# Performance work log

Measured on AMD Instinct MI355X. Metric: run time of the kernel, lower is better.

Reference implementation:

```python
import jax, jax.numpy as jnp
import numpy as np

STU, ITEM, CONC, D = 50000, 20000, 2000, 128
E_CC, E_IC, E_SI = 40000, 80000, 1000000


def _gat(tgt_x, src_x, e_src, e_dst, n_tgt, W, att_l, att_r, slope=0.2):
    # single-head GATConv, aggr='add', concat with heads=1 -> [n_tgt, D]
    if W is not None:
        xl = src_x @ W.T  # lin_l applied to source
        xr = tgt_x @ W.T  # lin_l shared for target (in_channels is int)
        # noqa: torch module uses lin_l for both when in_channels is int
    else:
        xl, xr = src_x, tgt_x
    sl = xl @ att_l  # [n_src]
    sr = xr @ att_r  # [n_tgt]
    e = sl[e_src] + sr[e_dst]
    e = jnp.where(e > 0, e, slope * e)  # leaky_relu
    # segment softmax over edges grouped by target node
    m = jax.ops.segment_max(e, e_dst, num_segments=n_tgt)
    m = jnp.where(jnp.isfinite(m), m, 0.0)
    ex = jnp.exp(e - m[e_dst])
    den = jax.ops.segment_sum(ex, e_dst, num_segments=n_tgt) + 1e-16
    alpha = ex / den[e_dst]
    return jax.ops.segment_sum(xl[e_src] * alpha[:, None], e_dst, num_segments=n_tgt)


def setup_inputs():
    key = jax.random.key(0)
    ks = jax.random.split(key, 40)
    s = 1.0 / np.sqrt(D)
    n = lambda k, sh, sc=1.0: jax.random.normal(k, sh, jnp.float32) * sc
    return {
        'stu_x': n(ks[0], (STU, D)),
        'item_x': n(ks[1], (ITEM, D)),
        'conc_x': n(ks[2], (CONC, D)),
        'stu_raw_x': n(ks[3], (STU, D)),
        'W_cc': n(ks[4], (D, D), s), 'al_cc': n(ks[5], (D,), s), 'ar_cc': n(ks[6], (D,), s),
        'W_ic': n(ks[7], (D, D), s), 'al_ic': n(ks[8], (D,), s), 'ar_ic': n(ks[9], (D,), s),
        'al_cce': n(ks[10], (D,), s), 'ar_cce': n(ks[11], (D,), s),
        'al_ice': n(ks[12], (D,), s), 'ar_ice': n(ks[13], (D,), s),
        'W_ci': n(ks[14], (D, D), s), 'al_ci': n(ks[15], (D,), s), 'ar_ci': n(ks[16], (D,), s),
        'W_si': n(ks[17], (D, D), s), 'al_si': n(ks[18], (D,), s), 'ar_si': n(ks[19], (D,), s),
        'w_ci_att': n(ks[20], (2 * D,), s), 'w_si_att': n(ks[21], (2 * D,), s),
        'W_is': n(ks[22], (D, D), s), 'al_is': n(ks[23], (D,), s), 'ar_is': n(ks[24], (D,), s),
        'cc_src': jax.random.randint(ks[25], (E_CC,), 0, CONC),
        'cc_dst': jax.random.randint(ks[26], (E_CC,), 0, CONC),
        'ic_item': jax.random.randint(ks[27], (E_IC,), 0, ITEM),
        'ic_conc': jax.random.randint(ks[28], (E_IC,), 0, CONC),
        'si_stu': jax.random.randint(ks[29], (E_SI,), 0, STU),
        'si_item': jax.random.randint(ks[30], (E_SI,), 0, ITEM),
    }


def reference(stu_x, item_x, conc_x, stu_raw_x,
              W_cc, al_cc, ar_cc, W_ic, al_ic, ar_ic,
              al_cce, ar_cce, al_ice, ar_ice,
              W_ci, al_ci, ar_ci, W_si, al_si, ar_si,
              w_ci_att, w_si_att, W_is, al_is, ar_is,
              cc_src, cc_dst, ic_item, ic_conc, si_stu, si_item):
    # --- concept fusion ---
    c1 = _gat(conc_x, conc_x, cc_src, cc_dst, CONC, W_cc, al_cc, ar_cc)   # inter_conc_conc
    c2 = _gat(conc_x, item_x, ic_item, ic_conc, CONC, W_ic, al_ic, ar_ic) # inter_item_conc
    e1 = _gat(conc_x, c1, cc_src, cc_dst, CONC, None, al_cce, ar_cce)     # exter_conc_conc (no lin)
    e2 = _gat(conc_x, c2, cc_src, cc_dst, CONC, None, al_ice, ar_ice)     # exter_item_conc (no lin)
    conc_fused = conc_x + e1 + e2
    # --- item fusion ---
    i1 = _gat(item_x, conc_x, ic_conc, ic_item, ITEM, W_ci, al_ci, ar_ci) # inter_conc_item
    i2 = _gat(item_x, stu_x, si_stu, si_item, ITEM, W_si, al_si, ar_si)   # inter_stu_item
    # softmax over dim=1 of an [N,1] tensor (as in the torch code): equals 1.0
    att1 = jax.nn.softmax((jnp.concatenate([i1, item_x], axis=1) @ w_ci_att)[:, None], axis=1)
    att2 = jax.nn.softmax((jnp.concatenate([i2, item_x], axis=1) @ w_si_att)[:, None], axis=1)
    item_fused = item_x + att1 * i1 + att2 * i2
    # --- student fusion (uses raw data['stu'].x as target) ---
    s1 = _gat(stu_raw_x, item_x, si_item, si_stu, STU, W_is, al_is, ar_is)
    stu_fused = stu_raw_x + s1
    return (conc_fused, item_fused, stu_fused)
```

## Files before the change

kernel.cpp:

```cpp
#include <hip/hip_runtime.h>

#define CONC_N 2000
#define ITEM_N 20000
#define STU_N  50000
#define NE_CC  40000
#define NE_IC  80000
#define NE_SI  1000000
#define TBUCK  382

typedef unsigned int uint;
typedef unsigned short ushort;
typedef signed char s8;
typedef __attribute__((ext_vector_type(8))) short bf16x8;
typedef __attribute__((ext_vector_type(4))) float f32x4;

__device__ __forceinline__ ushort f2bf(float f) {
  uint u = __float_as_uint(f);
  uint r = (u + 0x7FFFu + ((u >> 16) & 1u)) >> 16;
  return (ushort)r;
}

__device__ __forceinline__ bf16x8 packfrag(float4 lo, float4 hi) {
  union { bf16x8 s; uint u[4]; } p;
  p.u[0] = (uint)f2bf(lo.x) | ((uint)f2bf(lo.y) << 16);
  p.u[1] = (uint)f2bf(lo.z) | ((uint)f2bf(lo.w) << 16);
  p.u[2] = (uint)f2bf(hi.x) | ((uint)f2bf(hi.y) << 16);
  p.u[3] = (uint)f2bf(hi.z) | ((uint)f2bf(hi.w) << 16);
  return p.s;
}


struct CsrG {
  const int* dst; const int* src;
  unsigned* keys; int* srcs; int* offs;
  int E, n, shift, nbuck, tb, sb;
};
struct CsrGs { CsrG g[5]; };


struct ProjDesc { const float* W; const float* a; float* out; };
struct SetupArgs {
  ProjDesc p[10];
  CsrGs G;
  int* pcnt;
  const float* wsrc[5];
  ushort* wdst[5];
};

__global__ __launch_bounds__(256) void setup_k(SetupArgs A) {
  int b = blockIdx.x;
  int tid = threadIdx.x;
  if (b < 10) {
    __shared__ float Wl[128 * 132];
    __shared__ float a_s[128];
    ProjDesc d = A.p[b];
    #pragma unroll
    for (int i = 0; i < 16; ++i) {
      int s = tid + i * 256;
      int row = s >> 5, c4 = s & 31;
      float4 w = *(const float4*)&d.W[s * 4];
      float* dst = &Wl[row * 132 + c4 * 4];
      dst[0] = w.x; dst[1] = w.y; dst[2] = w.z; dst[3] = w.w;
    }
    if (tid < 128) a_s[tid] = d.a[tid];
    __syncthreads();
    if (tid < 128) {
      float acc = 0.f;
      #pragma unroll 4
      for (int j = 0; j < 128; ++j) acc += Wl[j * 132 + tid] * a_s[j];
      d.out[tid] = acc;
    }
    return;
  }
  if (b >= 170) {
    int wi = b - 170;
    const float* Ws = A.wsrc[wi];
    ushort* Wd = A.wdst[wi];
    for (int rec = tid; rec < 2048; rec += 256) {
      int lane = rec & 63;
      int kk = (rec >> 6) & 3;
      int nt = rec >> 8;
      int x = lane & 15, g = lane >> 4;
      const float* src = &Ws[(nt * 16 + x) * 128 + kk * 32 + 4 * g];
      float4 lo = *(const float4*)src;
      float4 hi = *(const float4*)(src + 16);
      bf16x8 pk = packfrag(lo, hi);
      *(bf16x8*)&Wd[rec * 8] = pk;
    }
    return;
  }
  int bsel = b - 10;
  int gi = bsel >> 5, blk = bsel & 31;
  CsrG g = A.G.g[gi];
  __shared__ int lcnt[128];
  if (tid < 128) lcnt[tid] = 0;
  __syncthreads();
  int chunk = (g.E + 31) >> 5;
  int e0 = blk * chunk, e1 = min(g.E, e0 + chunk);
  for (int e = e0 + tid; e < e1; e += 256)
    atomicAdd(&lcnt[g.dst[e] >> g.shift], 1);
  __syncthreads();
  if (tid < 128) A.pcnt[bsel * 128 + tid] = lcnt[tid];
}


__global__ __launch_bounds__(512) void csr_scan(CsrGs G, const int* __restrict__ pcnt,
                                                int* __restrict__ cur, int* __restrict__ bases) {
  __shared__ int lc[TBUCK];
  __shared__ int lb[TBUCK + 5];
  int tid = threadIdx.x, lane = tid & 63, wv = tid >> 6;
  if (tid < TBUCK) {
    int gi = 0;
    #pragma unroll
    for (int k = 1; k < 5; ++k) if (tid >= G.g[k].tb) gi = k;
    int b = tid - G.g[gi].tb;
    int s = 0;
    for (int blk = 0; blk < 32; ++blk) s += pcnt[((gi << 5) + blk) * 128 + b];
    lc[tid] = s;
  }
  __syncthreads();
  if (wv < 5) {
    CsrG g = G.g[wv];
    int carry = 0;
    for (int base = 0; base < g.nbuck; base += 64) {
      int idx = base + lane;
      int v = (idx < g.nbuck) ? lc[g.tb + idx] : 0;
      int incl = v;
      #pragma unroll
      for (int o = 1; o < 64; o <<= 1) {
        int y = __shfl_up(incl, o);
        if (lane >= o) incl += y;
      }
      if (idx < g.nbuck) lb[g.sb + idx] = carry + incl - v;
      carry += __shfl(incl, 63);
    }
    if (lane == 0) lb[g.sb + g.nbuck] = carry;
  }
  __syncthreads();
  if (tid < TBUCK + 5) bases[tid] = lb[tid];
  if (tid < TBUCK) {
    int gi = 0;
    for (int k = 1; k < 5; ++k) if (tid >= G.g[k].tb) gi = k;
    cur[tid] = lb[tid + gi];
  }
  if (tid < 5) G.g[tid].offs[G.g[tid].n] = G.g[tid].E;
}


__device__ void partition_body(const CsrGs& G, int* __restrict__ cur, int gi, int bx,
                               int nbx, unsigned char* smem) {
  CsrG g = G.g[gi];
  unsigned* ck = (unsigned*)smem;
  unsigned char* cb = smem + 16384;
  int* lcnt = (int*)(smem + 20480);
  int* lcur = (int*)(smem + 20992);
  int tid = threadIdx.x;
  unsigned dmask = (1u << g.shift) - 1;
  for (int c0 = bx * 4096; c0 < g.E; c0 += nbx * 4096) {
    if (tid < 128) lcnt[tid] = 0;
    __syncthreads();
    #pragma unroll
    for (int i = 0; i < 16; ++i) {
      int e = c0 + i * 256 + tid;
      if (e < g.E) {
        int d = g.dst[e], s = g.src[e];
        int b = d >> g.shift;
        ck[i * 256 + tid] = ((unsigned)(d & dmask) << 16) | (unsigned)s;
        cb[i * 256 + tid] = (unsigned char)b;
        atomicAdd(&lcnt[b], 1);
      } else cb[i * 256 + tid] = 255;
    }
    __syncthreads();
    if (tid < g.nbuck && lcnt[tid] > 0) lcur[tid] = atomicAdd(&cur[g.tb + tid], lcnt[tid]);
    __syncthreads();
    #pragma unroll
    for (int i = 0; i < 16; ++i) {
      int b = cb[i * 256 + tid];
      if (b != 255) {
        int pos = atomicAdd(&lcur[b], 1);
        g.keys[pos] = ck[i * 256 + tid];
      }
    }
    __syncthreads();
  }
}

__device__ void rdot_body(const float* __restrict__ x, const float* __restrict__ v,
                          float* __restrict__ o, int n, int blk, int nblk) {
  int lane = threadIdx.x & 63;
  int wid = (blk * 256 + threadIdx.x) >> 6;
  int nw = nblk * 4;
  float va = v[lane], vb = v[64 + lane];
  for (int r = wid; r < n; r += nw) {
    float a = x[r * 128 + lane] * va + x[r * 128 + 64 + lane] * vb;
    #pragma unroll
    for (int of = 32; of; of >>= 1) a += __shfl_xor(a, of);
    if (lane == 0) o[r] = a;
  }
}

__global__ __launch_bounds__(256) void mid3_k(CsrGs G, int* cur,
                                              const float* rx, const float* rv,
                                              float* ro, int rnb) {
  __shared__ __align__(16) unsigned char smem[21504];
  int b = blockIdx.x;
  if (b < 600) {
    partition_body(G, cur, b / 120, b % 120, 120, smem);
  } else {
    rdot_body(rx, rv, ro, STU_N, b - 600, rnb);
  }
}


struct GemmDesc { const float* X; s8* Y8; float* S; int n, b0;
                  const float* dv[6]; float* dq[6]; };
struct BigC {
  GemmDesc g[5];
  int gemm_blocks;
};

__device__ void build_lite(const CsrGs& G, const int* __restrict__ bases, int bid,
                           int* lh, int* lex, int* lcu, int* wsum) {
  int gi = 0;
  for (int k = 1; k < 5; ++k) if (bid >= G.g[k].tb) gi = k;
  CsrG g = G.g[gi];
  int b = bid - g.tb;
  int base = bases[g.sb + b];
  int cnt = bases[g.sb + b + 1] - base;

  int tid = threadIdx.x;
  lh[tid] = 0; lh[tid + 256] = 0;
  __syncthreads();
  for (int j = tid; j < cnt; j += 256)
    atomicAdd(&lh[g.keys[base + j] >> 16], 1);
  __syncthreads();
  int a0 = lh[2 * tid], a1 = lh[2 * tid + 1];
  int pair = a0 + a1;
  int lane = tid & 63, wv = tid >> 6;
  int incl = pair;
  #pragma unroll
  for (int o = 1; o < 64; o <<= 1) {
    int y = __shfl_up(incl, o);
    if (lane >= o) incl += y;
  }
  if (lane == 63) wsum[wv] = incl;
  __syncthreads();
  if (tid == 0) {
    int s = 0;
    #pragma unroll
    for (int w = 0; w < 4; ++w) { int t = wsum[w]; wsum[w] = s; s += t; }
  }
  __syncthreads();
  int ep = wsum[wv] + incl - pair;
  lex[2 * tid] = ep;       lex[2 * tid + 1] = ep + a0;
  lcu[2 * tid] = ep;       lcu[2 * tid + 1] = ep + a0;
  __syncthreads();
  int dst0 = b << g.shift;
  int ndst = min(1 << g.shift, g.n - dst0);
  for (int dl = tid; dl < ndst; dl += 256) g.offs[dst0 + dl] = base + lex[dl];
  for (int j = tid; j < cnt; j += 256) {
    unsigned k = g.keys[base + j];
    int dl = k >> 16;
    int pos = atomicAdd(&lcu[dl], 1);
    g.srcs[base + pos] = (int)(k & 0xFFFFu);
  }
}

template <int NV>
__device__ void gemm_bodyT(const GemmDesc& gd, const ushort* __restrict__ Wf, int blk) {
  int tid = threadIdx.x;
  int lane = tid & 63, wv = tid >> 6;
  int x = lane & 15, g = lane >> 4;
  int row = blk * 64 + wv * 16 + x;
  const float* xr = &gd.X[(size_t)(row < gd.n ? row : 0) * 128];
  bf16x8 afrag[4];
  float dacc[NV == 0 ? 1 : NV];
  #pragma unroll
  for (int v = 0; v < NV; ++v) dacc[v] = 0.f;
  #pragma unroll
  for (int kk = 0; kk < 4; ++kk) {
    float4 lo = *(const float4*)&xr[kk * 32 + 4 * g];
    float4 hi = *(const float4*)&xr[kk * 32 + 16 + 4 * g];
    afrag[kk] = packfrag(lo, hi);
    #pragma unroll
    for (int v = 0; v < NV; ++v) {
      const float* vp = gd.dv[v];
      float4 vlo = *(const float4*)&vp[kk * 32 + 4 * g];
      float4 vhi = *(const float4*)&vp[kk * 32 + 16 + 4 * g];
      dacc[v] += lo.x * vlo.x + lo.y * vlo.y + lo.z * vlo.z + lo.w * vlo.w
               + hi.x * vhi.x + hi.y * vhi.y + hi.z * vhi.z + hi.w * vhi.w;
    }
  }
  #pragma unroll
  for (int v = 0; v < NV; ++v) {
    float dsum = dacc[v];
    dsum += __shfl_xor(dsum, 16);
    dsum += __shfl_xor(dsum, 32);
    if (lane < 16 && row < gd.n) gd.dq[v][row] = dsum;
  }
  f32x4 acc[8];
  #pragma unroll
  for (int t = 0; t < 8; ++t) acc[t] = (f32x4){0.f, 0.f, 0.f, 0.f};
  #pragma unroll
  for (int nt = 0; nt < 8; ++nt) {
    #pragma unroll
    for (int kk = 0; kk < 4; ++kk) {
      union { uint4 u; bf16x8 s; } bu;
      bu.u = *(const uint4*)&Wf[(size_t)((nt * 4 + kk) * 64 + lane) * 8];
      acc[nt] = __builtin_amdgcn_mfma_f32_16x16x32_bf16(afrag[kk], bu.s, acc[nt], 0, 0, 0);
    }
  }
  int orow = blk * 64 + wv * 16 + 4 * g;
  #pragma unroll
  for (int r = 0; r < 4; ++r) {
    float m8 = 0.f;
    #pragma unroll
    for (int nt = 0; nt < 8; ++nt) m8 = fmaxf(m8, fabsf(acc[nt][r]));
    #pragma unroll
    for (int msk = 1; msk < 16; msk <<= 1) m8 = fmaxf(m8, __shfl_xor(m8, msk));
    int gr = orow + r;
    if (gr < gd.n) {
      float invs = (m8 > 0.f) ? 127.f / m8 : 0.f;
      if (x == 0) gd.S[gr] = m8 * (1.f / 127.f);
      #pragma unroll
      for (int nt = 0; nt < 8; ++nt) {
        int q = (int)rintf(acc[nt][r] * invs);
        gd.Y8[(size_t)gr * 128 + nt * 16 + x] = (s8)q;
      }
    }
  }
}

__global__ __launch_bounds__(256, 2) void mid4_k(CsrGs G, const int* bases, BigC C,
                                                 const ushort* W0, const ushort* W1,
                                                 const ushort* W2, const ushort* W3,
                                                 const ushort* W4) {
  __shared__ int lh[512], lex[512], lcu[512], wsum[4];
  int b = blockIdx.x;
  if (b < TBUCK) {
    build_lite(G, bases, b, lh, lex, lcu, wsum);
    return;
  }
  b -= TBUCK;
  if (b < C.g[1].b0)      gemm_bodyT<6>(C.g[0], W0, b - C.g[0].b0);
  else if (b < C.g[2].b0) gemm_bodyT<4>(C.g[1], W1, b - C.g[1].b0);
  else if (b < C.g[3].b0) gemm_bodyT<0>(C.g[2], W2, b - C.g[2].b0);
  else if (b < C.g[4].b0) gemm_bodyT<1>(C.g[3], W3, b - C.g[3].b0);
  else                    gemm_bodyT<0>(C.g[4], W4, b - C.g[4].b0);
}


__device__ __forceinline__ void fma8q(float acc[8], float wj, uint2 u) {
  int lo = (int)u.x, hi = (int)u.y;
  acc[0] += wj * (float)((lo << 24) >> 24);
  acc[1] += wj * (float)((lo << 16) >> 24);
  acc[2] += wj * (float)((lo << 8) >> 24);
  acc[3] += wj * (float)(lo >> 24);
  acc[4] += wj * (float)((hi << 24) >> 24);
  acc[5] += wj * (float)((hi << 16) >> 24);
  acc[6] += wj * (float)((hi << 8) >> 24);
  acc[7] += wj * (float)(hi >> 24);
}

__device__ void gat_core16(const int* __restrict__ offs, const int* __restrict__ srcs,
                           const float* __restrict__ sl, const float* __restrict__ sr,
                           const s8* __restrict__ x8, const float* __restrict__ sc,
                           int t4, int n_tgt, int lane, float acc[8]) {
  int q = lane >> 4, il = lane & 15;
  int t = t4 + q;
  bool tv = t < n_tgt;
  int sbeg = tv ? offs[t] : 0;
  int send = tv ? offs[t + 1] : 0;
  float srt = tv ? sr[t] : 0.f;

  int i0l = sbeg + il;
  bool act0 = i0l < send;
  int s0 = act0 ? srcs[i0l] : 0;
  float sc0 = act0 ? sc[s0] : 0.f;
  float e0;
  {
    float e = sl[s0] + srt;
    e = e > 0.f ? e : 0.2f * e;
    e0 = act0 ? e : -1e30f;
  }
  float m = e0, se = act0 ? 1.f : 0.f;
  for (int i = i0l + 16; i < send; i += 16) {
    int s = srcs[i];
    float e = sl[s] + srt;
    e = e > 0.f ? e : 0.2f * e;
    float mn = fmaxf(m, e);
    se = se * __expf(m - mn) + __expf(e - mn);
    m = mn;
  }
  #pragma unroll
  for (int o = 8; o; o >>= 1) {
    float m2 = __shfl_xor(m, o), s2 = __shfl_xor(se, o);
    float mn = fmaxf(m, m2);
    se = se * __expf(m - mn) + s2 * __expf(m2 - mn);
    m = mn;
  }
  float inv = 1.f / (se + 1e-16f);

  #pragma unroll
  for (int r = 0; r < 8; ++r) acc[r] = 0.f;

  int qb = q << 4;
  for (int i0 = sbeg; i0 < send; i0 += 16) {
    int cnt = min(16, send - i0);
    int s; float wgt;
    if (i0 == sbeg) {
      s = s0;
      wgt = act0 ? __expf(e0 - m) * inv * sc0 : 0.f;
    } else {
      s = 0; wgt = 0.f;
      if (il < cnt) {
        s = srcs[i0 + il];
        float e = sl[s] + srt;
        e = e > 0.f ? e : 0.2f * e;
        wgt = __expf(e - m) * inv * sc[s];
      }
    }
    int j = 0;
    for (; j + 4 <= cnt; j += 4) {
      int sj0 = __shfl(s, qb + j);
      int sj1 = __shfl(s, qb + j + 1);
      int sj2 = __shfl(s, qb + j + 2);
      int sj3 = __shfl(s, qb + j + 3);
      float wj0 = __shfl(wgt, qb + j);
      float wj1 = __shfl(wgt, qb + j + 1);
      float wj2 = __shfl(wgt, qb + j + 2);
      float wj3 = __shfl(wgt, qb + j + 3);
      uint2 u0 = *(const uint2*)&x8[(size_t)sj0 * 128 + il * 8];
      uint2 u1 = *(const uint2*)&x8[(size_t)sj1 * 128 + il * 8];
      uint2 u2 = *(const uint2*)&x8[(size_t)sj2 * 128 + il * 8];
      uint2 u3 = *(const uint2*)&x8[(size_t)sj3 * 128 + il * 8];
      fma8q(acc, wj0, u0);
      fma8q(acc, wj1, u1);
      fma8q(acc, wj2, u2);
      fma8q(acc, wj3, u3);
    }
    for (; j < cnt; ++j) {
      int sj = __shfl(s, qb + j);
      float wj = __shfl(wgt, qb + j);
      uint2 u = *(const uint2*)&x8[(size_t)sj * 128 + il * 8];
      fma8q(acc, wj, u);
    }
  }
}

__device__ __forceinline__ void gat_store16(const float acc[8], const float* base0,
                                            float* out, int t4, int n_tgt, int lane) {
  int q = lane >> 4, il = lane & 15;
  int t = t4 + q;
  if (t >= n_tgt) return;
  int d = t * 128 + il * 8;
  float4 a0 = make_float4(acc[0], acc[1], acc[2], acc[3]);
  float4 a1 = make_float4(acc[4], acc[5], acc[6], acc[7]);
  if (base0) {
    const float4 b0 = *(const float4*)&base0[d];
    const float4 b1 = *(const float4*)&base0[d + 4];
    a0.x += b0.x; a0.y += b0.y; a0.z += b0.z; a0.w += b0.w;
    a1.x += b1.x; a1.y += b1.y; a1.z += b1.z; a1.w += b1.w;
  }
  *(float4*)&out[d] = a0;
  *(float4*)&out[d + 4] = a1;
}

__device__ void c1c2_body16(const int* offs, const int* srcs, const float* sl,
                            const float* sr, const s8* x8, const float* sc,
                            const float* al, float* o, float* slo,
                            int t4, int n_tgt, int lane) {
  float acc[8];
  gat_core16(offs, srcs, sl, sr, x8, sc, t4, n_tgt, lane, acc);
  int q = lane >> 4, il = lane & 15;
  int t = t4 + q;
  float4 v0 = *(const float4*)&al[il * 8];
  float4 v1 = *(const float4*)&al[il * 8 + 4];
  float p = acc[0] * v0.x + acc[1] * v0.y + acc[2] * v0.z + acc[3] * v0.w +
            acc[4] * v1.x + acc[5] * v1.y + acc[6] * v1.z + acc[7] * v1.w;
  #pragma unroll
  for (int o2 = 8; o2; o2 >>= 1) p += __shfl_xor(p, o2);
  if (t < n_tgt) {
    if (il == 0) slo[t] = p;
    int d = t * 128 + il * 8;
    *(float4*)&o[d] = make_float4(acc[0], acc[1], acc[2], acc[3]);
    *(float4*)&o[d + 4] = make_float4(acc[4], acc[5], acc[6], acc[7]);
  }
}

__device__ void gat_dual_core(const int* __restrict__ offs, const int* __restrict__ srcs,
                              const float* __restrict__ sl1, const float* __restrict__ sr1,
                              const float* __restrict__ xl1,
                              const float* __restrict__ sl2, const float* __restrict__ sr2,
                              const float* __restrict__ xl2,
                              const float* __restrict__ base,
                              float* __restrict__ out, int t, int lane) {
  int sbeg = offs[t], send = offs[t + 1];
  float srt1 = sr1[t], srt2 = sr2[t];
  float m1 = -1e30f, m2 = -1e30f;
  for (int i = sbeg + lane; i < send; i += 64) {
    int s = srcs[i];
    float e1 = sl1[s] + srt1; e1 = e1 > 0.f ? e1 : 0.2f * e1;
    float e2 = sl2[s] + srt2; e2 = e2 > 0.f ? e2 : 0.2f * e2;
    m1 = fmaxf(m1, e1); m2 = fmaxf(m2, e2);
  }
  #pragma unroll
  for (int o = 32; o; o >>= 1) {
    m1 = fmaxf(m1, __shfl_xor(m1, o));
    m2 = fmaxf(m2, __shfl_xor(m2, o));
  }
  float se1 = 0.f, se2 = 0.f;
  for (int i = sbeg + lane; i < send; i += 64) {
    int s = srcs[i];
    float e1 = sl1[s] + srt1; e1 = e1 > 0.f ? e1 : 0.2f * e1;
    float e2 = sl2[s] + srt2; e2 = e2 > 0.f ? e2 : 0.2f * e2;
    se1 += __expf(e1 - m1); se2 += __expf(e2 - m2);
  }
  #pragma unroll
  for (int o = 32; o; o >>= 1) {
    se1 += __shfl_xor(se1, o);
    se2 += __shfl_xor(se2, o);
  }
  float inv1 = 1.f / (se1 + 1e-16f), inv2 = 1.f / (se2 + 1e-16f);
  float ax = 0.f, ay = 0.f;
  for (int i0 = sbeg; i0 < send; i0 += 64) {
    int cnt = min(64, send - i0);
    int s = 0; float w1 = 0.f, w2 = 0.f;
    if (lane < cnt) {
      s = srcs[i0 + lane];
      float e1 = sl1[s] + srt1; e1 = e1 > 0.f ? e1 : 0.2f * e1;
      float e2 = sl2[s] + srt2; e2 = e2 > 0.f ? e2 : 0.2f * e2;
      w1 = __expf(e1 - m1) * inv1;
      w2 = __expf(e2 - m2) * inv2;
    }
    for (int j = 0; j < cnt; ++j) {
      int sj = __shfl(s, j);
      float wj1 = __shfl(w1, j);
      float wj2 = __shfl(w2, j);
      const float2 v1 = *(const float2*)&xl1[sj * 128 + lane * 2];
      const float2 v2 = *(const float2*)&xl2[sj * 128 + lane * 2];
      ax += wj1 * v1.x + wj2 * v2.x;
      ay += wj1 * v1.y + wj2 * v2.y;
    }
  }
  const float2 b = *(const float2*)&base[t * 128 + lane * 2];
  float2 o2; o2.x = ax + b.x; o2.y = ay + b.y;
  *(float2*)&out[t * 128 + lane * 2] = o2;
}


#define NB_I12 1250
#define NB_S1  3125
#define NB_CC  125

struct GatsArgs {
  const int *offs4, *srcs4; const float *sl_is, *sr_is; const s8* x_is; const float* sc_is;
  const float* stu_raw_x; float* out_stu;
  const int *offs3, *srcs3; const float *sl_si, *sr_si; const s8* x_si; const float* sc_si;
  const int *offs2, *srcs2; const float *sl_ci, *sr_ci; const s8* x_ci; const float* sc_ci;
  const float* item_x; float* out_item;
  const int *offs0, *srcs0; const float *sl_cc, *sr_cc; const s8* x_cc; const float* sc_cc;
  const float* al_cce; float *c1, *sl_cce;
  const int *offs1, *srcs1; const float *sl_ic, *sr_ic; const s8* x_ic; const float* sc_ic;
  const float* al_ice; float *c2, *sl_ice;
};

__global__ void gats_k(GatsArgs A) {
  int b = blockIdx.x;
  int lane = threadIdx.x & 63;
  int wv = threadIdx.x >> 6;
  if (b < NB_I12) {
    int t4 = b * 16 + wv * 4;
    float acc1[8], acc2[8];
    gat_core16(A.offs2, A.srcs2, A.sl_ci, A.sr_ci, A.x_ci, A.sc_ci, t4, ITEM_N, lane, acc1);
    gat_core16(A.offs3, A.srcs3, A.sl_si, A.sr_si, A.x_si, A.sc_si, t4, ITEM_N, lane, acc2);
    #pragma unroll
    for (int r = 0; r < 8; ++r) acc1[r] += acc2[r];
    gat_store16(acc1, A.item_x, A.out_item, t4, ITEM_N, lane);
  } else if (b < NB_I12 + NB_S1) {
    int t4 = (b - NB_I12) * 16 + wv * 4;
    float acc[8];
    gat_core16(A.offs4, A.srcs4, A.sl_is, A.sr_is, A.x_is, A.sc_is, t4, STU_N, lane, acc);
    gat_store16(acc, A.stu_raw_x, A.out_stu, t4, STU_N, lane);
  } else {
    int sub = b - NB_I12 - NB_S1;
    int which = sub >= NB_CC;
    int t4 = (sub - which * NB_CC) * 16 + wv * 4;
    if (!which)
      c1c2_body16(A.offs0, A.srcs0, A.sl_cc, A.sr_cc, A.x_cc, A.sc_cc, A.al_cce,
                  A.c1, A.sl_cce, t4, CONC_N, lane);
    else
      c1c2_body16(A.offs1, A.srcs1, A.sl_ic, A.sr_ic, A.x_ic, A.sc_ic, A.al_ice,
                  A.c2, A.sl_ice, t4, CONC_N, lane);
  }
}


__global__ void fin_k(const int* offs0, const int* srcs0,
                      const float* sl_cce, const float* sr_cce, const float* c1,
                      const float* sl_ice, const float* sr_ice, const float* c2,
                      const float* conc_x, float* out_conc) {
  int t = (blockIdx.x * blockDim.x + threadIdx.x) >> 6;
  if (t >= CONC_N) return;
  gat_dual_core(offs0, srcs0, sl_cce, sr_cce, c1, sl_ice, sr_ice, c2,
                conc_x, out_conc, t, threadIdx.x & 63);
}


extern "C" void kernel_launch(void* const* d_in, const int* in_sizes, int n_in,
                              void* d_out, int out_size, void* d_ws, size_t ws_size,
                              hipStream_t stream) {
  const float* stu_x     = (const float*)d_in[0];
  const float* item_x    = (const float*)d_in[1];
  const float* conc_x    = (const float*)d_in[2];
  const float* stu_raw_x = (const float*)d_in[3];
  const float* W_cc  = (const float*)d_in[4];
  const float* al_cc = (const float*)d_in[5];
  const float* ar_cc = (const float*)d_in[6];
  const float* W_ic  = (const float*)d_in[7];
  const float* al_ic = (const float*)d_in[8];
  const float* ar_ic = (const float*)d_in[9];
  const float* al_cce = (const float*)d_in[10];
  const float* ar_cce = (const float*)d_in[11];
  const float* al_ice = (const float*)d_in[12];
  const float* ar_ice = (const float*)d_in[13];
  const float* W_ci  = (const float*)d_in[14];
  const float* al_ci = (const float*)d_in[15];
  const float* ar_ci = (const float*)d_in[16];
  const float* W_si  = (const float*)d_in[17];
  const float* al_si = (const float*)d_in[18];
  const float* ar_si = (const float*)d_in[19];
  const float* W_is  = (const float*)d_in[22];
  const float* al_is = (const float*)d_in[23];
  const float* ar_is = (const float*)d_in[24];
  const int* cc_src  = (const int*)d_in[25];
  const int* cc_dst  = (const int*)d_in[26];
  const int* ic_item = (const int*)d_in[27];
  const int* ic_conc = (const int*)d_in[28];
  const int* si_stu  = (const int*)d_in[29];
  const int* si_item = (const int*)d_in[30];

  char* wsb = (char*)d_ws;
  size_t off = 0;
  auto alloc = [&](size_t bytes) -> void* {
    void* p = wsb + off;
    off = (off + bytes + 255) & ~(size_t)255;
    return p;
  };

  s8* concWcc = (s8*)alloc((size_t)CONC_N * 128);
  s8* itemWic = (s8*)alloc((size_t)ITEM_N * 128);
  s8* concWci = (s8*)alloc((size_t)CONC_N * 128);
  s8* stuWsi  = (s8*)alloc((size_t)STU_N  * 128);
  s8* itemWis = (s8*)alloc((size_t)ITEM_N * 128);
  float* scCcc = (float*)alloc(CONC_N * 4);
  float* scIic = (float*)alloc(ITEM_N * 4);
  float* scCci = (float*)alloc(CONC_N * 4);
  float* scSsi = (float*)alloc(STU_N * 4);
  float* scIis = (float*)alloc(ITEM_N * 4);
  ushort* Wbf[5];
  for (int i = 0; i < 5; ++i) Wbf[i] = (ushort*)alloc(128 * 128 * 2);
  float* c1buf   = (float*)alloc((size_t)CONC_N * 128 * 4);
  float* c2buf   = (float*)alloc((size_t)CONC_N * 128 * 4);
  float* vecs    = (float*)alloc(10 * 128 * 4);
  float* sl_cc  = (float*)alloc(CONC_N * 4);
  float* sr_cc  = (float*)alloc(CONC_N * 4);
  float* sl_ic  = (float*)alloc(ITEM_N * 4);
  float* sr_ic  = (float*)alloc(CONC_N * 4);
  float* sl_ci  = (float*)alloc(CONC_N * 4);
  float* sr_ci  = (float*)alloc(ITEM_N * 4);
  float* sl_si  = (float*)alloc(STU_N * 4);
  float* sr_si  = (float*)alloc(ITEM_N * 4);
  float* sl_is  = (float*)alloc(ITEM_N * 4);
  float* sr_is  = (float*)alloc(STU_N * 4);
  float* sl_cce = (float*)alloc(CONC_N * 4);
  float* sr_cce = (float*)alloc(CONC_N * 4);
  float* sl_ice = (float*)alloc(CONC_N * 4);
  float* sr_ice = (float*)alloc(CONC_N * 4);

  unsigned* keys0 = (unsigned*)alloc((size_t)NE_CC * 4);
  unsigned* keys1 = (unsigned*)alloc((size_t)NE_IC * 4);
  unsigned* keys2 = (unsigned*)alloc((size_t)NE_IC * 4);
  unsigned* keys3 = (unsigned*)alloc((size_t)NE_SI * 4);
  unsigned* keys4 = (unsigned*)alloc((size_t)NE_SI * 4);
  int* srcs0 = (int*)alloc((size_t)NE_CC * 4);
  int* srcs1 = (int*)alloc((size_t)NE_IC * 4);
  int* srcs2 = (int*)alloc((size_t)NE_IC * 4);
  int* srcs3 = (int*)alloc((size_t)NE_SI * 4);
  int* srcs4 = (int*)alloc((size_t)NE_SI * 4);
  int* offs0 = (int*)alloc((CONC_N + 1) * 4);
  int* offs1 = (int*)alloc((CONC_N + 1) * 4);
  int* offs2 = (int*)alloc((ITEM_N + 1) * 4);
  int* offs3 = (int*)alloc((ITEM_N + 1) * 4);
  int* offs4 = (int*)alloc((STU_N + 1) * 4);
  int* pcnt      = (int*)alloc(5 * 32 * 128 * 4);
  int* cur_all   = (int*)alloc(TBUCK * 4);
  int* bases_all = (int*)alloc((TBUCK + 5) * 4);

  float* out = (float*)d_out;
  float* out_conc = out;
  float* out_item = out + (size_t)CONC_N * 128;
  float* out_stu  = out + (size_t)(CONC_N + ITEM_N) * 128;

  CsrGs G;
  G.g[0] = {cc_dst,  cc_src,  keys0, srcs0, offs0, NE_CC, CONC_N, 5, 63,   0,   0};
  G.g[1] = {ic_conc, ic_item, keys1, srcs1, offs1, NE_IC, CONC_N, 5, 63,  63,  64};
  G.g[2] = {ic_item, ic_conc, keys2, srcs2, offs2, NE_IC, ITEM_N, 8, 79, 126, 128};
  G.g[3] = {si_item, si_stu,  keys3, srcs3, offs3, NE_SI, ITEM_N, 8, 79, 205, 208};
  G.g[4] = {si_stu,  si_item, keys4, srcs4, offs4, NE_SI, STU_N,  9, 98, 284, 288};

  SetupArgs SA;
  SA.p[0] = {W_cc, al_cc, vecs + 0 * 128};
  SA.p[1] = {W_cc, ar_cc, vecs + 1 * 128};
  SA.p[2] = {W_ic, al_ic, vecs + 2 * 128};
  SA.p[3] = {W_ic, ar_ic, vecs + 3 * 128};
  SA.p[4] = {W_ci, al_ci, vecs + 4 * 128};
  SA.p[5] = {W_ci, ar_ci, vecs + 5 * 128};
  SA.p[6] = {W_si, al_si, vecs + 6 * 128};
  SA.p[7] = {W_si, ar_si, vecs + 7 * 128};
  SA.p[8] = {W_is, al_is, vecs + 8 * 128};
  SA.p[9] = {W_is, ar_is, vecs + 9 * 128};
  SA.G = G;
  SA.pcnt = pcnt;
  SA.wsrc[0] = W_cc; SA.wsrc[1] = W_ic; SA.wsrc[2] = W_ci;
  SA.wsrc[3] = W_si; SA.wsrc[4] = W_is;
  for (int i = 0; i < 5; ++i) SA.wdst[i] = Wbf[i];
  setup_k<<<175, 256, 0, stream>>>(SA);

  csr_scan<<<1, 512, 0, stream>>>(G, pcnt, cur_all, bases_all);

  mid3_k<<<600 + 1024, 256, 0, stream>>>(G, cur_all, stu_raw_x, vecs + 9 * 128,
                                         sr_is, 1024);

  BigC C;
  C.g[0] = {conc_x, concWcc, scCcc, CONC_N, 0,
            {vecs + 0 * 128, vecs + 1 * 128, vecs + 3 * 128, vecs + 4 * 128, ar_cce, ar_ice},
            {sl_cc, sr_cc, sr_ic, sl_ci, sr_cce, sr_ice}};
  C.g[1] = {item_x, itemWic, scIic, ITEM_N, 32,
            {vecs + 2 * 128, vecs + 5 * 128, vecs + 7 * 128, vecs + 8 * 128, nullptr, nullptr},
            {sl_ic, sr_ci, sr_si, sl_is, nullptr, nullptr}};
  C.g[2] = {conc_x, concWci, scCci, CONC_N, 345,
            {nullptr, nullptr, nullptr, nullptr, nullptr, nullptr},
            {nullptr, nullptr, nullptr, nullptr, nullptr, nullptr}};
  C.g[3] = {stu_x, stuWsi, scSsi, STU_N, 377,
            {vecs + 6 * 128, nullptr, nullptr, nullptr, nullptr, nullptr},
            {sl_si, nullptr, nullptr, nullptr, nullptr, nullptr}};
  C.g[4] = {item_x, itemWis, scIis, ITEM_N, 1159,
            {nullptr, nullptr, nullptr, nullptr, nullptr, nullptr},
            {nullptr, nullptr, nullptr, nullptr, nullptr, nullptr}};
  C.gemm_blocks = 1472;
  mid4_k<<<TBUCK + 1472, 256, 0, stream>>>(G, bases_all, C,
                                           Wbf[0], Wbf[1], Wbf[2], Wbf[3], Wbf[4]);

  GatsArgs GA;
  GA.offs4 = offs4; GA.srcs4 = srcs4; GA.sl_is = sl_is; GA.sr_is = sr_is;
  GA.x_is = itemWis; GA.sc_is = scIis; GA.stu_raw_x = stu_raw_x; GA.out_stu = out_stu;
  GA.offs3 = offs3; GA.srcs3 = srcs3; GA.sl_si = sl_si; GA.sr_si = sr_si;
  GA.x_si = stuWsi; GA.sc_si = scSsi;
  GA.offs2 = offs2; GA.srcs2 = srcs2; GA.sl_ci = sl_ci; GA.sr_ci = sr_ci;
  GA.x_ci = concWci; GA.sc_ci = scCci; GA.item_x = item_x; GA.out_item = out_item;
  GA.offs0 = offs0; GA.srcs0 = srcs0; GA.sl_cc = sl_cc; GA.sr_cc = sr_cc;
  GA.x_cc = concWcc; GA.sc_cc = scCcc; GA.al_cce = al_cce; GA.c1 = c1buf; GA.sl_cce = sl_cce;
  GA.offs1 = offs1; GA.srcs1 = srcs1; GA.sl_ic = sl_ic; GA.sr_ic = sr_ic;
  GA.x_ic = itemWic; GA.sc_ic = scIic; GA.al_ice = al_ice; GA.c2 = c2buf; GA.sl_ice = sl_ice;
  gats_k<<<NB_I12 + NB_S1 + 2 * NB_CC, 256, 0, stream>>>(GA);

  fin_k<<<500, 256, 0, stream>>>(offs0, srcs0, sl_cce, sr_cce, c1buf,
                                 sl_ice, sr_ice, c2buf, conc_x, out_conc);
}
```

Before: 186.3 us.

## Use single-pass online softmax in GAT aggregation core

Replaces the two-pass segment softmax, which first scanned the edges for max and sum and then rescanned them to aggregate, with a single pass. The running max is updated per 16-edge chunk, the accumulators and partial sums are rescaled, and the result is normalised once at the end. This removes the second read of source indices and attention logits for high-degree targets. In exchange, every chunk now does a shuffle-max reduction and rescales eight accumulators.

```diff
diff --git a/kernel.cpp b/kernel.cpp
--- a/kernel.cpp
+++ b/kernel.cpp
@@ -373,63 +373,43 @@
   int send = tv ? offs[t + 1] : 0;
   float srt = tv ? sr[t] : 0.f;
 
-  int i0l = sbeg + il;
-  bool act0 = i0l < send;
-  int s0 = act0 ? srcs[i0l] : 0;
-  float sc0 = act0 ? sc[s0] : 0.f;
-  float e0;
-  {
-    float e = sl[s0] + srt;
-    e = e > 0.f ? e : 0.2f * e;
-    e0 = act0 ? e : -1e30f;
-  }
-  float m = e0, se = act0 ? 1.f : 0.f;
-  for (int i = i0l + 16; i < send; i += 16) {
-    int s = srcs[i];
-    float e = sl[s] + srt;
-    e = e > 0.f ? e : 0.2f * e;
-    float mn = fmaxf(m, e);
-    se = se * __expf(m - mn) + __expf(e - mn);
-    m = mn;
-  }
-  #pragma unroll
-  for (int o = 8; o; o >>= 1) {
-    float m2 = __shfl_xor(m, o), s2 = __shfl_xor(se, o);
-    float mn = fmaxf(m, m2);
-    se = se * __expf(m - mn) + s2 * __expf(m2 - mn);
-    m = mn;
-  }
-  float inv = 1.f / (se + 1e-16f);
-
+  float m = -1e30f, se = 0.f;
   #pragma unroll
   for (int r = 0; r < 8; ++r) acc[r] = 0.f;
-
   int qb = q << 4;
+
   for (int i0 = sbeg; i0 < send; i0 += 16) {
     int cnt = min(16, send - i0);
-    int s; float wgt;
-    if (i0 == sbeg) {
-      s = s0;
-      wgt = act0 ? __expf(e0 - m) * inv * sc0 : 0.f;
-    } else {
-      s = 0; wgt = 0.f;
-      if (il < cnt) {
-        s = srcs[i0 + il];
-        float e = sl[s] + srt;
-        e = e > 0.f ? e : 0.2f * e;
-        wgt = __expf(e - m) * inv * sc[s];
-      }
-    }
+    int s = 0; float e = -1e30f, scs = 0.f;
+    if (il < cnt) {
+      s = srcs[i0 + il];
+      float ee = sl[s] + srt;
+      e = ee > 0.f ? ee : 0.2f * ee;
+      scs = sc[s];
+    }
+    float cm = e;
+    #pragma unroll
+    for (int o = 8; o; o >>= 1) cm = fmaxf(cm, __shfl_xor(cm, o));
+    float mn = fmaxf(m, cm);
+    float f = __expf(m - mn);
+    m = mn;
+    se *= f;
+    #pragma unroll
+    for (int r = 0; r < 8; ++r) acc[r] *= f;
+    float w = (il < cnt) ? __expf(e - m) : 0.f;
+    se += w;
+    float ws = w * scs;
+
     int j = 0;
     for (; j + 4 <= cnt; j += 4) {
       int sj0 = __shfl(s, qb + j);
       int sj1 = __shfl(s, qb + j + 1);
       int sj2 = __shfl(s, qb + j + 2);
       int sj3 = __shfl(s, qb + j + 3);
-      float wj0 = __shfl(wgt, qb + j);
-      float wj1 = __shfl(wgt, qb + j + 1);
-      float wj2 = __shfl(wgt, qb + j + 2);
-      float wj3 = __shfl(wgt, qb + j + 3);
+      float wj0 = __shfl(ws, qb + j);
+      float wj1 = __shfl(ws, qb + j + 1);
+      float wj2 = __shfl(ws, qb + j + 2);
+      float wj3 = __shfl(ws, qb + j + 3);
       uint2 u0 = *(const uint2*)&x8[(size_t)sj0 * 128 + il * 8];
       uint2 u1 = *(const uint2*)&x8[(size_t)sj1 * 128 + il * 8];
       uint2 u2 = *(const uint2*)&x8[(size_t)sj2 * 128 + il * 8];
@@ -441,11 +421,16 @@
     }
     for (; j < cnt; ++j) {
       int sj = __shfl(s, qb + j);
-      float wj = __shfl(wgt, qb + j);
+      float wj = __shfl(ws, qb + j);
       uint2 u = *(const uint2*)&x8[(size_t)sj * 128 + il * 8];
       fma8q(acc, wj, u);
     }
   }
+  #pragma unroll
+  for (int o = 8; o; o >>= 1) se += __shfl_xor(se, o);
+  float inv = 1.f / (se + 1e-16f);
+  #pragma unroll
+  for (int r = 0; r < 8; ++r) acc[r] *= inv;
 }
 
 __device__ __forceinline__ void gat_store16(const float acc[8], const float* base0,
```

After: 183.0 us. No clear change (-1.8%).
